# Kernel tuning notes

Hardware: AMD Instinct MI355X
Metric: run time of the kernel (lower is better)

The kernel has to match this reference:

```python
import jax, jax.numpy as jnp
import numpy as np

N = 50000   # nodes
E = 800000  # edges (avg degree 16)
IN = 3      # in_feats = value(1) + u(2)
H = 128     # hid_feats


def setup_inputs() -> dict:
    key = jax.random.key(0)
    ks = jax.random.split(key, 24)
    value = jax.random.normal(ks[0], (N, 1), jnp.float32)
    u = jax.random.normal(ks[1], (N, 2), jnp.float32)
    src = jax.random.randint(ks[2], (E,), 0, N, dtype=jnp.int32)
    dst = jax.random.randint(ks[3], (E,), 0, N, dtype=jnp.int32)
    dims = [IN, H // 2, H, H, H, H, H, H, H, H, 1]
    inp = {"value": value, "u": u, "src": src, "dst": dst}
    for i in range(10):
        inp[f"W{i+1}"] = jax.random.normal(ks[4 + i], (dims[i], dims[i + 1]), jnp.float32) / np.sqrt(dims[i]).astype(np.float32)
        inp[f"b{i+1}"] = jnp.zeros((dims[i + 1],), jnp.float32)
    return inp


def _gconv(x, src, dst, inv_deg, W, b):
    # DGL GraphConv norm='right': sum incoming src features, divide by in-degree, linear, bias
    agg = jax.ops.segment_sum(x[src], dst, num_segments=N)  # [N, d_in]
    return (agg * inv_deg) @ W + b


def reference(value, u, src, dst, W1, b1, W2, b2, W3, b3, W4, b4, W5, b5,
              W6, b6, W7, b7, W8, b8, W9, b9, W10, b10):
    deg = jax.ops.segment_sum(jnp.ones((E,), jnp.float32), dst, num_segments=N)
    inv_deg = (1.0 / jnp.clip(deg, 1.0))[:, None]  # DGL clamps in-degree to >=1
    lrelu = lambda h: jax.nn.leaky_relu(h, 0.01)
    x = jnp.concatenate([value, u], axis=1)  # [N, 3]
    h = _gconv(x, src, dst, inv_deg, W1, b1)
    h = lrelu(_gconv(h, src, dst, inv_deg, W2, b2))
    h = lrelu(_gconv(h, src, dst, inv_deg, W3, b3))
    h = lrelu(_gconv(h, src, dst, inv_deg, W4, b4))
    h = _gconv(h, src, dst, inv_deg, W5, b5)
    h = _gconv(h, src, dst, inv_deg, W6, b6)
    h = _gconv(h, src, dst, inv_deg, W7, b7)
    h = _gconv(h, src, dst, inv_deg, W8, b8)
    h = jax.nn.sigmoid(_gconv(h, src, dst, inv_deg, W9, b9))
    h = _gconv(h, src, dst, inv_deg, W10, b10)  # [N, 1]
    return h
```

## Files before the change

kernel.cpp:

```cpp
#include <hip/hip_runtime.h>
#include <math.h>

typedef unsigned int u32;
typedef unsigned short u16;
using bf16x8 = __attribute__((ext_vector_type(8))) short;
using f32x4 = __attribute__((ext_vector_type(4))) float;

__device__ inline float bf_lo(u32 v) { return __uint_as_float(v << 16); }
__device__ inline float bf_hi(u32 v) { return __uint_as_float(v & 0xFFFF0000u); }
__device__ inline u16 f2bf(float f) {
    u32 u = __float_as_uint(f);
    return (u16)((u + 0x7FFFu + ((u >> 16) & 1u)) >> 16);
}
__device__ inline float bf2f(u16 h) { return __uint_as_float((u32)h << 16); }
__device__ inline float invdeg(int d) { return 1.0f / (float)(d > 1 ? d : 1); }

__global__ __launch_bounds__(256) void k_scatter_pad(const int* __restrict__ src,
                                                     const int* __restrict__ dst,
                                                     int* __restrict__ cur,
                                                     u16* __restrict__ colp, int E) {
    int e = blockIdx.x * 256 + threadIdx.x;
    if (e >= E) return;
    int d = dst[e];
    int slot = atomicAdd(&cur[d], 1);
    if (slot < 64) colp[(size_t)d * 64 + slot] = (u16)src[e];
}

__global__ __launch_bounds__(256) void k_x4(const float* __restrict__ value,
                                            const float* __restrict__ u,
                                            float4* __restrict__ x4, int n) {
    int i = blockIdx.x * 256 + threadIdx.x;
    if (i < n) x4[i] = make_float4(value[i], u[2 * i], u[2 * i + 1], 0.f);
}

struct W7 { const float* p[7]; };

__global__ __launch_bounds__(256) void k_pack(W7 wp, const float* __restrict__ W64,
                                              u16* __restrict__ hi128, u16* __restrict__ lo128,
                                              u16* __restrict__ hi64, u16* __restrict__ lo64) {
    const int l = blockIdx.y;
    if (l < 7) {
        const float* W = wp.p[l];
        int g = blockIdx.x * 256 + threadIdx.x;
        int ct = g >> 8;
        int rem = g & 255;
        int ks = rem >> 6;
        int lane = rem & 63;
        int kbase = ks * 32 + ((lane >> 4) << 3);
        int n = (ct << 4) + (lane & 15);
        size_t off = ((size_t)l * 2048 + g) * 8;
#pragma unroll
        for (int j = 0; j < 8; ++j) {
            float w = W[(size_t)(kbase + j) * 128 + n];
            u16 h = f2bf(w);
            hi128[off + j] = h;
            lo128[off + j] = f2bf(w - bf2f(h));
        }
    } else {
        if (blockIdx.x >= 4) return;
        int g = blockIdx.x * 256 + threadIdx.x;
        int ct = g >> 7;
        int rem = g & 127;
        int ks = rem >> 6;
        int lane = rem & 63;
        int kbase = ks * 32 + ((lane >> 4) << 3);
        int n = (ct << 4) + (lane & 15);
        size_t off = (size_t)g * 8;
#pragma unroll
        for (int j = 0; j < 8; ++j) {
            float w = W64[(size_t)(kbase + j) * 128 + n];
            u16 h = f2bf(w);
            hi64[off + j] = h;
            lo64[off + j] = f2bf(w - bf2f(h));
        }
    }
}

__global__ __launch_bounds__(256) void k_l1(const float4* __restrict__ x4,
                                            const u16* __restrict__ colp,
                                            const int* __restrict__ deg,
                                            const float* __restrict__ W1,
                                            const float* __restrict__ b1,
                                            u16* __restrict__ out, int nNodes) {
    const int lane = threadIdx.x & 63;
    const int n = blockIdx.x * 4 + (threadIdx.x >> 6);
    if (n >= nNodes) return;
    int dfull = deg[n];
    int dg = dfull > 64 ? 64 : dfull;
    const u16* cl = colp + (size_t)n * 64;
    float a0 = 0.f, a1 = 0.f, a2 = 0.f;
    if (lane < dg) {
        float4 v = x4[cl[lane]];
        a0 = v.x; a1 = v.y; a2 = v.z;
    }
#pragma unroll
    for (int o = 32; o; o >>= 1) {
        a0 += __shfl_xor(a0, o, 64);
        a1 += __shfl_xor(a1, o, 64);
        a2 += __shfl_xor(a2, o, 64);
    }
    float iv = invdeg(dfull);
    float y = b1[lane] + iv * (a0 * W1[lane] + a1 * W1[64 + lane] + a2 * W1[128 + lane]);
    out[(size_t)n * 64 + lane] = f2bf(y);
}

__global__ __launch_bounds__(256) void k_agg128b(const u32* __restrict__ H32,
                                                 const u16* __restrict__ colp,
                                                 const int* __restrict__ deg,
                                                 u32* __restrict__ out, int nNodes) {
    const int lane = threadIdx.x & 63;
    const int n = blockIdx.x * 4 + (threadIdx.x >> 6);
    if (n >= nNodes) return;
    int dfull = deg[n];
    int dg = dfull > 64 ? 64 : dfull;
    const u16* cl = colp + (size_t)n * 64;
    int myc = (lane < dg) ? (int)cl[lane] : 0;
    float a0 = 0.f, a1 = 0.f, b0 = 0.f, b1 = 0.f;
    int j = 0;
    for (; j + 8 <= dg; j += 8) {
        u32 v0 = H32[(size_t)__builtin_amdgcn_readlane(myc, j + 0) * 64 + lane];
        u32 v1 = H32[(size_t)__builtin_amdgcn_readlane(myc, j + 1) * 64 + lane];
        u32 v2 = H32[(size_t)__builtin_amdgcn_readlane(myc, j + 2) * 64 + lane];
        u32 v3 = H32[(size_t)__builtin_amdgcn_readlane(myc, j + 3) * 64 + lane];
        u32 v4 = H32[(size_t)__builtin_amdgcn_readlane(myc, j + 4) * 64 + lane];
        u32 v5 = H32[(size_t)__builtin_amdgcn_readlane(myc, j + 5) * 64 + lane];
        u32 v6 = H32[(size_t)__builtin_amdgcn_readlane(myc, j + 6) * 64 + lane];
        u32 v7 = H32[(size_t)__builtin_amdgcn_readlane(myc, j + 7) * 64 + lane];
        a0 += bf_lo(v0) + bf_lo(v1) + bf_lo(v2) + bf_lo(v3);
        a1 += bf_hi(v0) + bf_hi(v1) + bf_hi(v2) + bf_hi(v3);
        b0 += bf_lo(v4) + bf_lo(v5) + bf_lo(v6) + bf_lo(v7);
        b1 += bf_hi(v4) + bf_hi(v5) + bf_hi(v6) + bf_hi(v7);
    }
    for (; j + 4 <= dg; j += 4) {
        u32 v0 = H32[(size_t)__builtin_amdgcn_readlane(myc, j + 0) * 64 + lane];
        u32 v1 = H32[(size_t)__builtin_amdgcn_readlane(myc, j + 1) * 64 + lane];
        u32 v2 = H32[(size_t)__builtin_amdgcn_readlane(myc, j + 2) * 64 + lane];
        u32 v3 = H32[(size_t)__builtin_amdgcn_readlane(myc, j + 3) * 64 + lane];
        a0 += bf_lo(v0) + bf_lo(v1);
        a1 += bf_hi(v0) + bf_hi(v1);
        b0 += bf_lo(v2) + bf_lo(v3);
        b1 += bf_hi(v2) + bf_hi(v3);
    }
    for (; j < dg; ++j) {
        u32 v = H32[(size_t)__builtin_amdgcn_readlane(myc, j) * 64 + lane];
        a0 += bf_lo(v);
        a1 += bf_hi(v);
    }
    float iv = invdeg(dfull);
    out[(size_t)n * 64 + lane] =
        (u32)f2bf((a0 + b0) * iv) | ((u32)f2bf((a1 + b1) * iv) << 16);
}

__global__ __launch_bounds__(256) void k_agg64b(const u16* __restrict__ H16,
                                                const u16* __restrict__ colp,
                                                const int* __restrict__ deg,
                                                u16* __restrict__ out, int nNodes) {
    const int lane = threadIdx.x & 63;
    const int n = blockIdx.x * 4 + (threadIdx.x >> 6);
    if (n >= nNodes) return;
    int dfull = deg[n];
    int dg = dfull > 64 ? 64 : dfull;
    const u16* cl = colp + (size_t)n * 64;
    int myc = (lane < dg) ? (int)cl[lane] : 0;
    float a0 = 0.f, a1 = 0.f, b0 = 0.f, b1 = 0.f;
    int j = 0;
    for (; j + 8 <= dg; j += 8) {
        u16 v0 = H16[(size_t)__builtin_amdgcn_readlane(myc, j + 0) * 64 + lane];
        u16 v1 = H16[(size_t)__builtin_amdgcn_readlane(myc, j + 1) * 64 + lane];
        u16 v2 = H16[(size_t)__builtin_amdgcn_readlane(myc, j + 2) * 64 + lane];
        u16 v3 = H16[(size_t)__builtin_amdgcn_readlane(myc, j + 3) * 64 + lane];
        u16 v4 = H16[(size_t)__builtin_amdgcn_readlane(myc, j + 4) * 64 + lane];
        u16 v5 = H16[(size_t)__builtin_amdgcn_readlane(myc, j + 5) * 64 + lane];
        u16 v6 = H16[(size_t)__builtin_amdgcn_readlane(myc, j + 6) * 64 + lane];
        u16 v7 = H16[(size_t)__builtin_amdgcn_readlane(myc, j + 7) * 64 + lane];
        a0 += bf2f(v0) + bf2f(v1);
        a1 += bf2f(v2) + bf2f(v3);
        b0 += bf2f(v4) + bf2f(v5);
        b1 += bf2f(v6) + bf2f(v7);
    }
    for (; j + 4 <= dg; j += 4) {
        u16 v0 = H16[(size_t)__builtin_amdgcn_readlane(myc, j + 0) * 64 + lane];
        u16 v1 = H16[(size_t)__builtin_amdgcn_readlane(myc, j + 1) * 64 + lane];
        u16 v2 = H16[(size_t)__builtin_amdgcn_readlane(myc, j + 2) * 64 + lane];
        u16 v3 = H16[(size_t)__builtin_amdgcn_readlane(myc, j + 3) * 64 + lane];
        a0 += bf2f(v0) + bf2f(v1);
        b0 += bf2f(v2) + bf2f(v3);
    }
    for (; j < dg; ++j) {
        a0 += bf2f(H16[(size_t)__builtin_amdgcn_readlane(myc, j) * 64 + lane]);
    }
    out[(size_t)n * 64 + lane] = f2bf((a0 + a1 + b0 + b1) * invdeg(dfull));
}

template <int ACT>
__device__ inline float actf(float x) {
    if (ACT == 1) return x > 0.f ? x : 0.01f * x;
    if (ACT == 2) return 1.f / (1.f + expf(-x));
    return x;
}

template <int DIN, int ACT>
__global__ __launch_bounds__(256) void k_mm(const u16* __restrict__ A,
                                            const u16* __restrict__ pkHi,
                                            const u16* __restrict__ pkLo,
                                            const float* __restrict__ B,
                                            u16* __restrict__ Y, int nNodes) {
    constexpr int NKS = DIN / 32;
    const int lane = threadIdx.x & 63;
    const int w = threadIdx.x >> 6;
    const int base = blockIdx.x * 64 + w * 16;
    const int m = lane & 15;
    const int kb = lane >> 4;
    int arow = base + m;
    if (arow >= nNodes) arow = nNodes - 1;

    bf16x8 aF[NKS];
#pragma unroll
    for (int ks = 0; ks < NKS; ++ks)
        aF[ks] = *reinterpret_cast<const bf16x8*>(A + (size_t)arow * DIN + ks * 32 + kb * 8);

    const bf16x8* bh = reinterpret_cast<const bf16x8*>(pkHi);
    const bf16x8* bl = reinterpret_cast<const bf16x8*>(pkLo);

#pragma unroll
    for (int ct = 0; ct < 8; ++ct) {
        f32x4 acc = {0.f, 0.f, 0.f, 0.f};
#pragma unroll
        for (int ks = 0; ks < NKS; ++ks) {
            acc = __builtin_amdgcn_mfma_f32_16x16x32_bf16(aF[ks], bh[(ct * NKS + ks) * 64 + lane], acc, 0, 0, 0);
            acc = __builtin_amdgcn_mfma_f32_16x16x32_bf16(aF[ks], bl[(ct * NKS + ks) * 64 + lane], acc, 0, 0, 0);
        }
        float bias = B[ct * 16 + m];
#pragma unroll
        for (int r = 0; r < 4; ++r) {
            int row = base + kb * 4 + r;
            if (row < nNodes)
                Y[(size_t)row * 128 + ct * 16 + m] = f2bf(actf<ACT>(acc[r] + bias));
        }
    }
}

__global__ __launch_bounds__(256) void k_mm_last(const u16* __restrict__ A,
                                                 const u16* __restrict__ pkHi,
                                                 const u16* __restrict__ pkLo,
                                                 const float* __restrict__ B,
                                                 const float* __restrict__ w10,
                                                 float* __restrict__ t, int nNodes) {
    const int lane = threadIdx.x & 63;
    const int w = threadIdx.x >> 6;
    const int base = blockIdx.x * 64 + w * 16;
    const int m = lane & 15;
    const int kb = lane >> 4;
    int arow = base + m;
    if (arow >= nNodes) arow = nNodes - 1;

    bf16x8 aF[4];
#pragma unroll
    for (int ks = 0; ks < 4; ++ks)
        aF[ks] = *reinterpret_cast<const bf16x8*>(A + (size_t)arow * 128 + ks * 32 + kb * 8);

    const bf16x8* bh = reinterpret_cast<const bf16x8*>(pkHi);
    const bf16x8* bl = reinterpret_cast<const bf16x8*>(pkLo);

    float p0 = 0.f, p1 = 0.f, p2 = 0.f, p3 = 0.f;
#pragma unroll
    for (int ct = 0; ct < 8; ++ct) {
        f32x4 acc = {0.f, 0.f, 0.f, 0.f};
#pragma unroll
        for (int ks = 0; ks < 4; ++ks) {
            acc = __builtin_amdgcn_mfma_f32_16x16x32_bf16(aF[ks], bh[(ct * 4 + ks) * 64 + lane], acc, 0, 0, 0);
            acc = __builtin_amdgcn_mfma_f32_16x16x32_bf16(aF[ks], bl[(ct * 4 + ks) * 64 + lane], acc, 0, 0, 0);
        }
        float bias = B[ct * 16 + m];
        float wv = w10[ct * 16 + m];
        p0 += wv * actf<2>(acc[0] + bias);
        p1 += wv * actf<2>(acc[1] + bias);
        p2 += wv * actf<2>(acc[2] + bias);
        p3 += wv * actf<2>(acc[3] + bias);
    }
#pragma unroll
    for (int o = 1; o < 16; o <<= 1) {
        p0 += __shfl_xor(p0, o, 64);
        p1 += __shfl_xor(p1, o, 64);
        p2 += __shfl_xor(p2, o, 64);
        p3 += __shfl_xor(p3, o, 64);
    }
    if (m == 0) {
        int r0 = base + kb * 4;
        if (r0 + 0 < nNodes) t[r0 + 0] = p0;
        if (r0 + 1 < nNodes) t[r0 + 1] = p1;
        if (r0 + 2 < nNodes) t[r0 + 2] = p2;
        if (r0 + 3 < nNodes) t[r0 + 3] = p3;
    }
}

__global__ __launch_bounds__(256) void k_aggs(const float* __restrict__ t,
                                              const u16* __restrict__ colp,
                                              const int* __restrict__ deg,
                                              const float* __restrict__ B,
                                              float* __restrict__ out, int nNodes) {
    int n = blockIdx.x * 256 + threadIdx.x;
    if (n >= nNodes) return;
    int dfull = deg[n];
    int dg = dfull > 64 ? 64 : dfull;
    const u16* cl = colp + (size_t)n * 64;
    float s = 0.f;
    for (int j = 0; j < dg; ++j) s += t[cl[j]];
    out[n] = s * invdeg(dfull) + B[0];
}

extern "C" void kernel_launch(void* const* d_in, const int* in_sizes, int n_in,
                              void* d_out, int out_size, void* d_ws, size_t ws_size,
                              hipStream_t stream) {
    const float* value = (const float*)d_in[0];
    const float* u = (const float*)d_in[1];
    const int* src = (const int*)d_in[2];
    const int* dst = (const int*)d_in[3];
    const float* W[10];
    const float* b[10];
    for (int i = 0; i < 10; ++i) {
        W[i] = (const float*)d_in[4 + 2 * i];
        b[i] = (const float*)d_in[5 + 2 * i];
    }
    const int N = in_sizes[0];
    const int E = in_sizes[2];
    float* out = (float*)d_out;

    char* p = (char*)d_ws;
    auto carve = [&](size_t bytes) {
        char* r = p;
        p += (bytes + 255) & ~(size_t)255;
        return r;
    };
    int* deg = (int*)carve((size_t)N * 4);
    u16* colp = (u16*)carve((size_t)N * 64 * 2);
    float4* x4 = (float4*)carve((size_t)N * 16);
    u16* hA = (u16*)carve((size_t)N * 128 * 2);
    u16* hB = (u16*)carve((size_t)N * 128 * 2);
    u16* agg = (u16*)carve((size_t)N * 128 * 2);
    float* t10 = (float*)carve((size_t)N * 4);
    u16* pk128hi = (u16*)carve((size_t)7 * 2048 * 8 * 2);
    u16* pk128lo = (u16*)carve((size_t)7 * 2048 * 8 * 2);
    u16* pk64hi = (u16*)carve((size_t)1024 * 8 * 2);
    u16* pk64lo = (u16*)carve((size_t)1024 * 8 * 2);

    hipMemsetAsync(deg, 0, (size_t)N * 4, stream);
    k_scatter_pad<<<(E + 255) / 256, 256, 0, stream>>>(src, dst, deg, colp, E);
    k_x4<<<(N + 255) / 256, 256, 0, stream>>>(value, u, x4, N);

    W7 wp;
    for (int i = 0; i < 7; ++i) wp.p[i] = W[2 + i];
    k_pack<<<dim3(8, 8), 256, 0, stream>>>(wp, W[1], pk128hi, pk128lo, pk64hi, pk64lo);

    const int gw = (N + 3) / 4;
    const int gg = (N + 63) / 64;
    const int gt = (N + 255) / 256;
    const size_t PK = 2048 * 8;

    k_l1<<<gw, 256, 0, stream>>>(x4, colp, deg, W[0], b[0], hA, N);
    k_agg64b<<<gw, 256, 0, stream>>>(hA, colp, deg, agg, N);
    k_mm<64, 1><<<gg, 256, 0, stream>>>(agg, pk64hi, pk64lo, b[1], hB, N);
    k_agg128b<<<gw, 256, 0, stream>>>((const u32*)hB, colp, deg, (u32*)agg, N);
    k_mm<128, 1><<<gg, 256, 0, stream>>>(agg, pk128hi + 0 * PK, pk128lo + 0 * PK, b[2], hA, N);
    k_agg128b<<<gw, 256, 0, stream>>>((const u32*)hA, colp, deg, (u32*)agg, N);
    k_mm<128, 1><<<gg, 256, 0, stream>>>(agg, pk128hi + 1 * PK, pk128lo + 1 * PK, b[3], hB, N);
    k_agg128b<<<gw, 256, 0, stream>>>((const u32*)hB, colp, deg, (u32*)agg, N);
    k_mm<128, 0><<<gg, 256, 0, stream>>>(agg, pk128hi + 2 * PK, pk128lo + 2 * PK, b[4], hA, N);
    k_agg128b<<<gw, 256, 0, stream>>>((const u32*)hA, colp, deg, (u32*)agg, N);
    k_mm<128, 0><<<gg, 256, 0, stream>>>(agg, pk128hi + 3 * PK, pk128lo + 3 * PK, b[5], hB, N);
    k_agg128b<<<gw, 256, 0, stream>>>((const u32*)hB, colp, deg, (u32*)agg, N);
    k_mm<128, 0><<<gg, 256, 0, stream>>>(agg, pk128hi + 4 * PK, pk128lo + 4 * PK, b[6], hA, N);
    k_agg128b<<<gw, 256, 0, stream>>>((const u32*)hA, colp, deg, (u32*)agg, N);
    k_mm<128, 0><<<gg, 256, 0, stream>>>(agg, pk128hi + 5 * PK, pk128lo + 5 * PK, b[7], hB, N);
    k_agg128b<<<gw, 256, 0, stream>>>((const u32*)hB, colp, deg, (u32*)agg, N);
    k_mm_last<<<gg, 256, 0, stream>>>(agg, pk128hi + 6 * PK, pk128lo + 6 * PK, b[8], W[9], t10, N);
    k_aggs<<<gt, 256, 0, stream>>>(t10, colp, deg, b[9], out, N);
}
```

Baseline: 435.1 us.

## Bin edge scatter by destination range and double rows per MFMA wave

The edge scatter now runs as a 2D grid where each y-slice handles only edges whose destination falls in one 8192-node range. This keeps atomic counters and column writes local, aiming for better cache behaviour, at the cost of re-reading dst once per bin. The dense matmul kernels now process 32 rows per wave using two accumulators, so each loaded weight fragment is reused twice. This halves B-fragment traffic per row but raises register pressure and halves the grid size.

```diff
diff --git a/kernel.cpp b/kernel.cpp
--- a/kernel.cpp
+++ b/kernel.cpp
@@ -15,13 +15,17 @@
 __device__ inline float bf2f(u16 h) { return __uint_as_float((u32)h << 16); }
 __device__ inline float invdeg(int d) { return 1.0f / (float)(d > 1 ? d : 1); }
 
-__global__ __launch_bounds__(256) void k_scatter_pad(const int* __restrict__ src,
+#define BIN_SHIFT 13
+
+__global__ __launch_bounds__(256) void k_scatter_bin(const int* __restrict__ src,
                                                      const int* __restrict__ dst,
                                                      int* __restrict__ cur,
                                                      u16* __restrict__ colp, int E) {
+    const int bin = blockIdx.y;
     int e = blockIdx.x * 256 + threadIdx.x;
     if (e >= E) return;
     int d = dst[e];
+    if ((d >> BIN_SHIFT) != bin) return;
     int slot = atomicAdd(&cur[d], 1);
     if (slot < 64) colp[(size_t)d * 64 + slot] = (u16)src[e];
 }
@@ -208,34 +212,45 @@
     constexpr int NKS = DIN / 32;
     const int lane = threadIdx.x & 63;
     const int w = threadIdx.x >> 6;
-    const int base = blockIdx.x * 64 + w * 16;
+    const int base = blockIdx.x * 128 + w * 32;
     const int m = lane & 15;
     const int kb = lane >> 4;
-    int arow = base + m;
-    if (arow >= nNodes) arow = nNodes - 1;
-
-    bf16x8 aF[NKS];
-#pragma unroll
-    for (int ks = 0; ks < NKS; ++ks)
-        aF[ks] = *reinterpret_cast<const bf16x8*>(A + (size_t)arow * DIN + ks * 32 + kb * 8);
+
+    bf16x8 aF[2][NKS];
+#pragma unroll
+    for (int rb = 0; rb < 2; ++rb) {
+        int arow = base + rb * 16 + m;
+        if (arow >= nNodes) arow = nNodes - 1;
+#pragma unroll
+        for (int ks = 0; ks < NKS; ++ks)
+            aF[rb][ks] = *reinterpret_cast<const bf16x8*>(A + (size_t)arow * DIN + ks * 32 + kb * 8);
+    }
 
     const bf16x8* bh = reinterpret_cast<const bf16x8*>(pkHi);
     const bf16x8* bl = reinterpret_cast<const bf16x8*>(pkLo);
 
 #pragma unroll
     for (int ct = 0; ct < 8; ++ct) {
-        f32x4 acc = {0.f, 0.f, 0.f, 0.f};
+        f32x4 acc0 = {0.f, 0.f, 0.f, 0.f};
+        f32x4 acc1 = {0.f, 0.f, 0.f, 0.f};
 #pragma unroll
         for (int ks = 0; ks < NKS; ++ks) {
-            acc = __builtin_amdgcn_mfma_f32_16x16x32_bf16(aF[ks], bh[(ct * NKS + ks) * 64 + lane], acc, 0, 0, 0);
-            acc = __builtin_amdgcn_mfma_f32_16x16x32_bf16(aF[ks], bl[(ct * NKS + ks) * 64 + lane], acc, 0, 0, 0);
+            bf16x8 h = bh[(ct * NKS + ks) * 64 + lane];
+            bf16x8 l = bl[(ct * NKS + ks) * 64 + lane];
+            acc0 = __builtin_amdgcn_mfma_f32_16x16x32_bf16(aF[0][ks], h, acc0, 0, 0, 0);
+            acc0 = __builtin_amdgcn_mfma_f32_16x16x32_bf16(aF[0][ks], l, acc0, 0, 0, 0);
+            acc1 = __builtin_amdgcn_mfma_f32_16x16x32_bf16(aF[1][ks], h, acc1, 0, 0, 0);
+            acc1 = __builtin_amdgcn_mfma_f32_16x16x32_bf16(aF[1][ks], l, acc1, 0, 0, 0);
         }
         float bias = B[ct * 16 + m];
 #pragma unroll
         for (int r = 0; r < 4; ++r) {
-            int row = base + kb * 4 + r;
-            if (row < nNodes)
-                Y[(size_t)row * 128 + ct * 16 + m] = f2bf(actf<ACT>(acc[r] + bias));
+            int row0 = base + kb * 4 + r;
+            if (row0 < nNodes)
+                Y[(size_t)row0 * 128 + ct * 16 + m] = f2bf(actf<ACT>(acc0[r] + bias));
+            int row1 = base + 16 + kb * 4 + r;
+            if (row1 < nNodes)
+                Y[(size_t)row1 * 128 + ct * 16 + m] = f2bf(actf<ACT>(acc1[r] + bias));
         }
     }
 }
@@ -248,49 +263,62 @@
                                                  float* __restrict__ t, int nNodes) {
     const int lane = threadIdx.x & 63;
     const int w = threadIdx.x >> 6;
-    const int base = blockIdx.x * 64 + w * 16;
+    const int base = blockIdx.x * 128 + w * 32;
     const int m = lane & 15;
     const int kb = lane >> 4;
-    int arow = base + m;
-    if (arow >= nNodes) arow = nNodes - 1;
-
-    bf16x8 aF[4];
-#pragma unroll
-    for (int ks = 0; ks < 4; ++ks)
-        aF[ks] = *reinterpret_cast<const bf16x8*>(A + (size_t)arow * 128 + ks * 32 + kb * 8);
+
+    bf16x8 aF[2][4];
+#pragma unroll
+    for (int rb = 0; rb < 2; ++rb) {
+        int arow = base + rb * 16 + m;
+        if (arow >= nNodes) arow = nNodes - 1;
+#pragma unroll
+        for (int ks = 0; ks < 4; ++ks)
+            aF[rb][ks] = *reinterpret_cast<const bf16x8*>(A + (size_t)arow * 128 + ks * 32 + kb * 8);
+    }
 
     const bf16x8* bh = reinterpret_cast<const bf16x8*>(pkHi);
     const bf16x8* bl = reinterpret_cast<const bf16x8*>(pkLo);
 
-    float p0 = 0.f, p1 = 0.f, p2 = 0.f, p3 = 0.f;
+    float p0[4] = {0.f, 0.f, 0.f, 0.f};
+    float p1[4] = {0.f, 0.f, 0.f, 0.f};
 #pragma unroll
     for (int ct = 0; ct < 8; ++ct) {
-        f32x4 acc = {0.f, 0.f, 0.f, 0.f};
+        f32x4 acc0 = {0.f, 0.f, 0.f, 0.f};
+        f32x4 acc1 = {0.f, 0.f, 0.f, 0.f};
 #pragma unroll
         for (int ks = 0; ks < 4; ++ks) {
-            acc = __builtin_amdgcn_mfma_f32_16x16x32_bf16(aF[ks], bh[(ct * 4 + ks) * 64 + lane], acc, 0, 0, 0);
-            acc = __builtin_amdgcn_mfma_f32_16x16x32_bf16(aF[ks], bl[(ct * 4 + ks) * 64 + lane], acc, 0, 0, 0);
+            bf16x8 h = bh[(ct * 4 + ks) * 64 + lane];
+            bf16x8 l = bl[(ct * 4 + ks) * 64 + lane];
+            acc0 = __builtin_amdgcn_mfma_f32_16x16x32_bf16(aF[0][ks], h, acc0, 0, 0, 0);
+            acc0 = __builtin_amdgcn_mfma_f32_16x16x32_bf16(aF[0][ks], l, acc0, 0, 0, 0);
+            acc1 = __builtin_amdgcn_mfma_f32_16x16x32_bf16(aF[1][ks], h, acc1, 0, 0, 0);
+            acc1 = __builtin_amdgcn_mfma_f32_16x16x32_bf16(aF[1][ks], l, acc1, 0, 0, 0);
         }
         float bias = B[ct * 16 + m];
         float wv = w10[ct * 16 + m];
-        p0 += wv * actf<2>(acc[0] + bias);
-        p1 += wv * actf<2>(acc[1] + bias);
-        p2 += wv * actf<2>(acc[2] + bias);
-        p3 += wv * actf<2>(acc[3] + bias);
+#pragma unroll
+        for (int r = 0; r < 4; ++r) {
+            p0[r] += wv * actf<2>(acc0[r] + bias);
+            p1[r] += wv * actf<2>(acc1[r] + bias);
+        }
     }
 #pragma unroll
     for (int o = 1; o < 16; o <<= 1) {
-        p0 += __shfl_xor(p0, o, 64);
-        p1 += __shfl_xor(p1, o, 64);
-        p2 += __shfl_xor(p2, o, 64);
-        p3 += __shfl_xor(p3, o, 64);
+#pragma unroll
+        for (int r = 0; r < 4; ++r) {
+            p0[r] += __shfl_xor(p0[r], o, 64);
+            p1[r] += __shfl_xor(p1[r], o, 64);
+        }
     }
     if (m == 0) {
-        int r0 = base + kb * 4;
-        if (r0 + 0 < nNodes) t[r0 + 0] = p0;
-        if (r0 + 1 < nNodes) t[r0 + 1] = p1;
-        if (r0 + 2 < nNodes) t[r0 + 2] = p2;
-        if (r0 + 3 < nNodes) t[r0 + 3] = p3;
+#pragma unroll
+        for (int r = 0; r < 4; ++r) {
+            int row0 = base + kb * 4 + r;
+            if (row0 < nNodes) t[row0] = p0[r];
+            int row1 = base + 16 + kb * 4 + r;
+            if (row1 < nNodes) t[row1] = p1[r];
+        }
     }
 }
 
@@ -344,8 +372,10 @@
     u16* pk64hi = (u16*)carve((size_t)1024 * 8 * 2);
     u16* pk64lo = (u16*)carve((size_t)1024 * 8 * 2);
 
+    const int nbins = (N + (1 << BIN_SHIFT) - 1) >> BIN_SHIFT;
+
     hipMemsetAsync(deg, 0, (size_t)N * 4, stream);
-    k_scatter_pad<<<(E + 255) / 256, 256, 0, stream>>>(src, dst, deg, colp, E);
+    k_scatter_bin<<<dim3((E + 255) / 256, nbins), 256, 0, stream>>>(src, dst, deg, colp, E);
     k_x4<<<(N + 255) / 256, 256, 0, stream>>>(value, u, x4, N);
 
     W7 wp;
@@ -353,26 +383,26 @@
     k_pack<<<dim3(8, 8), 256, 0, stream>>>(wp, W[1], pk128hi, pk128lo, pk64hi, pk64lo);
 
     const int gw = (N + 3) / 4;
-    const int gg = (N + 63) / 64;
+    const int gm = (N + 127) / 128;
     const int gt = (N + 255) / 256;
     const size_t PK = 2048 * 8;
 
     k_l1<<<gw, 256, 0, stream>>>(x4, colp, deg, W[0], b[0], hA, N);
     k_agg64b<<<gw, 256, 0, stream>>>(hA, colp, deg, agg, N);
-    k_mm<64, 1><<<gg, 256, 0, stream>>>(agg, pk64hi, pk64lo, b[1], hB, N);
+    k_mm<64, 1><<<gm, 256, 0, stream>>>(agg, pk64hi, pk64lo, b[1], hB, N);
     k_agg128b<<<gw, 256, 0, stream>>>((const u32*)hB, colp, deg, (u32*)agg, N);
-    k_mm<128, 1><<<gg, 256, 0, stream>>>(agg, pk128hi + 0 * PK, pk128lo + 0 * PK, b[2], hA, N);
+    k_mm<128, 1><<<gm, 256, 0, stream>>>(agg, pk128hi + 0 * PK, pk128lo + 0 * PK, b[2], hA, N);
     k_agg128b<<<gw, 256, 0, stream>>>((const u32*)hA, colp, deg, (u32*)agg, N);
-    k_mm<128, 1><<<gg, 256, 0, stream>>>(agg, pk128hi + 1 * PK, pk128lo + 1 * PK, b[3], hB, N);
+    k_mm<128, 1><<<gm, 256, 0, stream>>>(agg, pk128hi + 1 * PK, pk128lo + 1 * PK, b[3], hB, N);
     k_agg128b<<<gw, 256, 0, stream>>>((const u32*)hB, colp, deg, (u32*)agg, N);
-    k_mm<128, 0><<<gg, 256, 0, stream>>>(agg, pk128hi + 2 * PK, pk128lo + 2 * PK, b[4], hA, N);
+    k_mm<128, 0><<<gm, 256, 0, stream>>>(agg, pk128hi + 2 * PK, pk128lo + 2 * PK, b[4], hA, N);
     k_agg128b<<<gw, 256, 0, stream>>>((const u32*)hA, colp, deg, (u32*)agg, N);
-    k_mm<128, 0><<<gg, 256, 0, stream>>>(agg, pk128hi + 3 * PK, pk128lo + 3 * PK, b[5], hB, N);
+    k_mm<128, 0><<<gm, 256, 0, stream>>>(agg, pk128hi + 3 * PK, pk128lo + 3 * PK, b[5], hB, N);
     k_agg128b<<<gw, 256, 0, stream>>>((const u32*)hB, colp, deg, (u32*)agg, N);
-    k_mm<128, 0><<<gg, 256, 0, stream>>>(agg, pk128hi + 4 * PK, pk128lo + 4 * PK, b[6], hA, N);
+    k_mm<128, 0><<<gm, 256, 0, stream>>>(agg, pk128hi + 4 * PK, pk128lo + 4 * PK, b[6], hA, N);
     k_agg128b<<<gw, 256, 0, stream>>>((const u32*)hA, colp, deg, (u32*)agg, N);
-    k_mm<128, 0><<<gg, 256, 0, stream>>>(agg, pk128hi + 5 * PK, pk128lo + 5 * PK, b[7], hB, N);
+    k_mm<128, 0><<<gm, 256, 0, stream>>>(agg, pk128hi + 5 * PK, pk128lo + 5 * PK, b[7], hB, N);
     k_agg128b<<<gw, 256, 0, stream>>>((const u32*)hB, colp, deg, (u32*)agg, N);
-    k_mm_last<<<gg, 256, 0, stream>>>(agg, pk128hi + 6 * PK, pk128lo + 6 * PK, b[8], W[9], t10, N);
+    k_mm_last<<<gm, 256, 0, stream>>>(agg, pk128hi + 6 * PK, pk128lo + 6 * PK, b[8], W[9], t10, N);
     k_aggs<<<gt, 256, 0, stream>>>(t10, colp, deg, b[9], out, N);
 }
```

After: 444.4 us. 1.02x slower.
